# Performance work log

Measured on AMD Instinct MI355X. Metric: run time of the kernel, lower is better.

Reference implementation:

```python
import jax, jax.numpy as jnp
import numpy as np

ROUTING_ITERS = 3
EPS = 1e-8


def squash(x):
    # scale = ||x||^2 / (1 + ||x||^2); out = scale * x / (||x|| + eps)
    norm = jnp.linalg.norm(x, axis=-1, keepdims=True)
    scale = norm ** 2 / (1.0 + norm ** 2)
    return scale * x / (norm + EPS)


def setup_inputs() -> dict:
    key = jax.random.key(0)
    kx, kw = jax.random.split(key)
    B, R, C, IC, OC = 256, 1152, 10, 8, 16
    x = jax.random.normal(kx, (B, R, IC), dtype=jnp.float32)
    # learned prediction weights: [1, num_routes, num_capsules, in_ch, out_ch]
    weights = jax.random.normal(kw, (1, R, C, IC, OC), dtype=jnp.float32)
    return {"x": x, "weights": weights}


def reference(x, weights):
    # prediction vectors u_hat[b,r,c,o] = sum_i x[b,r,i] * W[r,c,i,o]
    u = jnp.einsum('bri,rcio->brco', x, weights[0])  # [B,R,C,OC]
    b = jnp.zeros(u.shape[:3], dtype=u.dtype)        # routing logits [B,R,C]
    v = jnp.zeros(u.shape[:1] + u.shape[2:], dtype=u.dtype)
    for _ in range(ROUTING_ITERS):
        c = jax.nn.softmax(b, axis=-1)               # coupling coeffs over capsules
        s = jnp.einsum('brc,brco->bco', c, u)        # weighted sum over routes
        v = squash(s)                                # [B,C,OC]
        b = b + jnp.einsum('brco,bco->brc', u, v)    # agreement update
    return v
```

## Files before the change

kernel.cpp:

```cpp
#include <hip/hip_runtime.h>
#include <cstdint>
#include <cstddef>

#define NB 256
#define NR 1152
#define NC 10
#define NI 8
#define NO 16
#define NSPLIT 2
#define NSWEEP 9
#define NRC 144

static __device__ __forceinline__ uint32_t bf16_pack2(float lo, float hi) {
    uint32_t vl = __float_as_uint(lo);
    vl = vl + 0x7FFFu + ((vl >> 16) & 1u);
    uint32_t vh = __float_as_uint(hi);
    vh = vh + 0x7FFFu + ((vh >> 16) & 1u);
    return (vl >> 16) | (vh & 0xFFFF0000u);
}

__global__ __launch_bounds__(320, 2) void caps_u_s1_kernel(
    const float* __restrict__ x, const float* __restrict__ W,
    uint32_t* __restrict__ u, uint32_t* __restrict__ part1)
{
    const int t  = threadIdx.x;
    const int c  = t >> 5;
    const int rl = (t & 31) >> 2;
    const int oq = t & 3;
    const int rc = blockIdx.x >> 4;
    const int bg = blockIdx.x & 15;
    const int b0 = bg * 16;
    const int r  = rc * 8 + rl;

    __shared__ float xs[16][8][8];

    if (t < 256) {
        const int bi = t >> 4, rem = t & 15;
        const int rr = rem >> 1, hf = rem & 1;
        *(float4*)&xs[bi][rr][hf * 4] =
            *(const float4*)(x + ((size_t)(b0 + bi) * NR + rc * 8 + rr) * 8 + hf * 4);
    }

    const float* wb = W + ((size_t)r * NC + c) * (NI * NO) + oq * 4;
    float4 wf[8];
#pragma unroll
    for (int i = 0; i < 8; ++i) wf[i] = *(const float4*)(wb + i * NO);

    __syncthreads();

#pragma unroll 2
    for (int bi = 0; bi < 16; ++bi) {
        const float4 xv4a = *(const float4*)&xs[bi][rl][0];
        const float4 xv4b = *(const float4*)&xs[bi][rl][4];
        const float xr[8] = {xv4a.x, xv4a.y, xv4a.z, xv4a.w,
                             xv4b.x, xv4b.y, xv4b.z, xv4b.w};
        float ax = 0.f, ay = 0.f, az = 0.f, aw = 0.f;
#pragma unroll
        for (int i = 0; i < 8; ++i) {
            const float xv = xr[i];
            ax = fmaf(xv, wf[i].x, ax); ay = fmaf(xv, wf[i].y, ay);
            az = fmaf(xv, wf[i].z, az); aw = fmaf(xv, wf[i].w, aw);
        }
        uint2 s;
        s.x = bf16_pack2(ax, ay);
        s.y = bf16_pack2(az, aw);
        *(uint2*)(u + (((size_t)(b0 + bi) * NC + c) * NR + r) * 8 + oq * 2) = s;

        float sx = ax, sy = ay, sz = az, sw = aw;
#pragma unroll
        for (int off = 4; off <= 16; off <<= 1) {
            sx += __shfl_xor(sx, off); sy += __shfl_xor(sy, off);
            sz += __shfl_xor(sz, off); sw += __shfl_xor(sw, off);
        }
        if ((t & 28) == 0) {
            uint2 p;
            p.x = bf16_pack2(sx, sy);
            p.y = bf16_pack2(sz, sw);
            *(uint2*)(part1 + ((size_t)(b0 + bi) * NRC + rc) * 80
                      + c * 8 + oq * 2) = p;
        }
    }
}

static __device__ __forceinline__ float vsum1_col(
    const uint32_t* __restrict__ part1, const int b, const int t)
{
    const uint32_t* p = part1 + (size_t)b * NRC * 80 + (t >> 1);
    const bool hi = t & 1;
    float s0 = 0.f, s1 = 0.f, s2 = 0.f, s3 = 0.f;
#pragma unroll 4
    for (int g = 0; g < NRC; g += 4) {
        const uint32_t w0 = p[(g + 0) * 80];
        const uint32_t w1 = p[(g + 1) * 80];
        const uint32_t w2 = p[(g + 2) * 80];
        const uint32_t w3 = p[(g + 3) * 80];
        s0 += hi ? __uint_as_float(w0 & 0xFFFF0000u) : __uint_as_float(w0 << 16);
        s1 += hi ? __uint_as_float(w1 & 0xFFFF0000u) : __uint_as_float(w1 << 16);
        s2 += hi ? __uint_as_float(w2 & 0xFFFF0000u) : __uint_as_float(w2 << 16);
        s3 += hi ? __uint_as_float(w3 & 0xFFFF0000u) : __uint_as_float(w3 << 16);
    }
    const float s = 0.1f * ((s0 + s1) + (s2 + s3));
    float n2 = s * s;
    n2 += __shfl_xor(n2, 1);
    n2 += __shfl_xor(n2, 2);
    n2 += __shfl_xor(n2, 4);
    n2 += __shfl_xor(n2, 8);
    const float nrm   = sqrtf(n2);
    return s * (n2 / (1.f + n2) / (nrm + 1e-8f));
}

__global__ __launch_bounds__(256, 2) void caps_pass_kernel(
    const uint32_t* __restrict__ u, const uint32_t* __restrict__ part1,
    const float* __restrict__ part_prev, float* __restrict__ partout)
{
    const int b  = blockIdx.x >> 1;
    const int sp = blockIdx.x & 1;
    const int t  = threadIdx.x;
    const int oq = t & 3;
    const int rl = t >> 2;

    __shared__ float vss[160];
    __shared__ float sred[4][160];

    if (t < 160) {
        float v = vsum1_col(part1, b, t);
        if (part_prev != nullptr) {
            const float s = part_prev[(size_t)b * 160 + t]
                          + part_prev[((size_t)NB + b) * 160 + t];
            float n2 = s * s;
            n2 += __shfl_xor(n2, 1);
            n2 += __shfl_xor(n2, 2);
            n2 += __shfl_xor(n2, 4);
            n2 += __shfl_xor(n2, 8);
            const float nrm = sqrtf(n2);
            v += s * (n2 / (1.f + n2) / (nrm + 1e-8f));
        }
        vss[t] = v;
    }
    __syncthreads();

    float acc[10][4];
#pragma unroll
    for (int c = 0; c < 10; ++c)
#pragma unroll
        for (int j = 0; j < 4; ++j) acc[c][j] = 0.f;

    const uint2* ub = (const uint2*)u + (size_t)b * NC * NR * 4 + oq;

    for (int k = 0; k < NSWEEP; ++k) {
        const int r = sp * (NSWEEP * 64) + k * 64 + rl;
        uint2 q[10];
#pragma unroll
        for (int c = 0; c < 10; ++c) q[c] = ub[((size_t)c * NR + r) * 4];

        float lg[10];
#pragma unroll
        for (int c = 0; c < 10; ++c) {
            const float4 vq = *(const float4*)&vss[c * 16 + oq * 4];
            float d = __uint_as_float(q[c].x << 16) * vq.x;
            d = fmaf(__uint_as_float(q[c].x & 0xFFFF0000u), vq.y, d);
            d = fmaf(__uint_as_float(q[c].y << 16),         vq.z, d);
            d = fmaf(__uint_as_float(q[c].y & 0xFFFF0000u), vq.w, d);
            lg[c] = d;
        }
#pragma unroll
        for (int c = 0; c < 10; ++c) {
            lg[c] += __shfl_xor(lg[c], 1);
            lg[c] += __shfl_xor(lg[c], 2);
        }
        float m = lg[0];
#pragma unroll
        for (int c = 1; c < 10; ++c) m = fmaxf(m, lg[c]);
        float wgt[10], ssum = 0.f;
#pragma unroll
        for (int c = 0; c < 10; ++c) { wgt[c] = __expf(lg[c] - m); ssum += wgt[c]; }
        const float inv = 1.f / ssum;
#pragma unroll
        for (int c = 0; c < 10; ++c) {
            const float wv = wgt[c] * inv;
            acc[c][0] = fmaf(wv, __uint_as_float(q[c].x << 16),         acc[c][0]);
            acc[c][1] = fmaf(wv, __uint_as_float(q[c].x & 0xFFFF0000u), acc[c][1]);
            acc[c][2] = fmaf(wv, __uint_as_float(q[c].y << 16),         acc[c][2]);
            acc[c][3] = fmaf(wv, __uint_as_float(q[c].y & 0xFFFF0000u), acc[c][3]);
        }
    }

#pragma unroll
    for (int off = 4; off <= 32; off <<= 1)
#pragma unroll
        for (int c = 0; c < 10; ++c)
#pragma unroll
            for (int j = 0; j < 4; ++j) acc[c][j] += __shfl_xor(acc[c][j], off);

    const int wv = t >> 6;
    if ((t & 63) < 4) {
#pragma unroll
        for (int c = 0; c < 10; ++c)
#pragma unroll
            for (int j = 0; j < 4; ++j)
                sred[wv][c * 16 + oq * 4 + j] = acc[c][j];
    }
    __syncthreads();

    if (t < 160) {
        partout[((size_t)sp * NB + b) * 160 + t]
            = sred[0][t] + sred[1][t] + sred[2][t] + sred[3][t];
    }
}

__global__ __launch_bounds__(192) void caps_final_kernel(
    const float* __restrict__ part2b, float* __restrict__ out)
{
    const int b = blockIdx.x;
    const int t = threadIdx.x;
    if (t >= 160) return;
    const float s = part2b[(size_t)b * 160 + t]
                  + part2b[((size_t)NB + b) * 160 + t];
    float n2 = s * s;
    n2 += __shfl_xor(n2, 1);
    n2 += __shfl_xor(n2, 2);
    n2 += __shfl_xor(n2, 4);
    n2 += __shfl_xor(n2, 8);
    const float nrm   = sqrtf(n2);
    const float scale = n2 / (1.f + n2) / (nrm + 1e-8f);
    out[(size_t)b * 160 + t] = scale * s;
}

extern "C" void kernel_launch(void* const* d_in, const int* in_sizes, int n_in,
                              void* d_out, int out_size, void* d_ws, size_t ws_size,
                              hipStream_t stream) {
    const float* x = (const float*)d_in[0];
    const float* W = (const float*)d_in[1];
    float* out = (float*)d_out;

    uint8_t*  ws   = (uint8_t*)d_ws;
    uint32_t* u    = (uint32_t*)ws;
    uint32_t* prt1 = (uint32_t*)(ws + 94371840u);
    float*    p2a  = (float*)(ws + 94371840u + 11796480u);
    float*    p2b  = (float*)(ws + 94371840u + 11796480u + 327680u);

    caps_u_s1_kernel<<<2304, 320, 0, stream>>>(x, W, u, prt1);
    caps_pass_kernel<<<NB * NSPLIT, 256, 0, stream>>>(u, prt1, nullptr, p2a);
    caps_pass_kernel<<<NB * NSPLIT, 256, 0, stream>>>(u, prt1, p2a, p2b);
    caps_final_kernel<<<NB, 192, 0, stream>>>(p2b, out);
}
```

Measured before the change: 142.8 us.

## Split routing passes six ways per batch and stage u slice in LDS

The routing pass kernels now split each batch's 1152 routes across six blocks of 192 routes instead of two blocks of 576. Each block first bulk-loads its bf16 u slice into shared memory with wide vector loads, then reads it from LDS in the sweep loop. This raises the block count to improve GPU fill and latency hiding on the memory-bound passes. In exchange it adds 60KB of LDS per block, which limits occupancy, and triples the partial-sum reduction work in the consumers.

```diff
diff --git a/kernel.cpp b/kernel.cpp
--- a/kernel.cpp
+++ b/kernel.cpp
@@ -7,8 +7,8 @@
 #define NC 10
 #define NI 8
 #define NO 16
-#define NSPLIT 2
-#define NSWEEP 9
+#define NSPLIT 6
+#define RPB 192
 #define NRC 144
 
 static __device__ __forceinline__ uint32_t bf16_pack2(float lo, float hi) {
@@ -105,7 +105,7 @@
     n2 += __shfl_xor(n2, 2);
     n2 += __shfl_xor(n2, 4);
     n2 += __shfl_xor(n2, 8);
-    const float nrm   = sqrtf(n2);
+    const float nrm = sqrtf(n2);
     return s * (n2 / (1.f + n2) / (nrm + 1e-8f));
 }
 
@@ -113,20 +113,35 @@
     const uint32_t* __restrict__ u, const uint32_t* __restrict__ part1,
     const float* __restrict__ part_prev, float* __restrict__ partout)
 {
-    const int b  = blockIdx.x >> 1;
-    const int sp = blockIdx.x & 1;
+    const int b  = blockIdx.x / NSPLIT;
+    const int sp = blockIdx.x % NSPLIT;
     const int t  = threadIdx.x;
     const int oq = t & 3;
     const int rl = t >> 2;
 
+    __shared__ uint32_t lds_u[15360];
     __shared__ float vss[160];
     __shared__ float sred[4][160];
+
+    {
+        const uint4* gsrc = (const uint4*)u;
+#pragma unroll
+        for (int j = 0; j < 15; ++j) {
+            const int f  = j * 256 + t;
+            const int c  = f / 384;
+            const int ro = f - c * 384;
+            const uint4 v = gsrc[((size_t)(b * NC + c) * NR + sp * RPB) * 2 + ro];
+            *(uint4*)&lds_u[(size_t)f * 4] = v;
+        }
+    }
 
     if (t < 160) {
         float v = vsum1_col(part1, b, t);
         if (part_prev != nullptr) {
-            const float s = part_prev[(size_t)b * 160 + t]
-                          + part_prev[((size_t)NB + b) * 160 + t];
+            float s = 0.f;
+#pragma unroll
+            for (int sp2 = 0; sp2 < NSPLIT; ++sp2)
+                s += part_prev[((size_t)sp2 * NB + b) * 160 + t];
             float n2 = s * s;
             n2 += __shfl_xor(n2, 1);
             n2 += __shfl_xor(n2, 2);
@@ -145,13 +160,12 @@
 #pragma unroll
         for (int j = 0; j < 4; ++j) acc[c][j] = 0.f;
 
-    const uint2* ub = (const uint2*)u + (size_t)b * NC * NR * 4 + oq;
-
-    for (int k = 0; k < NSWEEP; ++k) {
-        const int r = sp * (NSWEEP * 64) + k * 64 + rl;
+    for (int k = 0; k < 3; ++k) {
+        const int r = k * 64 + rl;
         uint2 q[10];
 #pragma unroll
-        for (int c = 0; c < 10; ++c) q[c] = ub[((size_t)c * NR + r) * 4];
+        for (int c = 0; c < 10; ++c)
+            q[c] = *(const uint2*)&lds_u[c * 1536 + r * 8 + oq * 2];
 
         float lg[10];
 #pragma unroll
@@ -214,8 +228,10 @@
     const int b = blockIdx.x;
     const int t = threadIdx.x;
     if (t >= 160) return;
-    const float s = part2b[(size_t)b * 160 + t]
-                  + part2b[((size_t)NB + b) * 160 + t];
+    float s = 0.f;
+#pragma unroll
+    for (int sp = 0; sp < NSPLIT; ++sp)
+        s += part2b[((size_t)sp * NB + b) * 160 + t];
     float n2 = s * s;
     n2 += __shfl_xor(n2, 1);
     n2 += __shfl_xor(n2, 2);
@@ -237,7 +253,7 @@
     uint32_t* u    = (uint32_t*)ws;
     uint32_t* prt1 = (uint32_t*)(ws + 94371840u);
     float*    p2a  = (float*)(ws + 94371840u + 11796480u);
-    float*    p2b  = (float*)(ws + 94371840u + 11796480u + 327680u);
+    float*    p2b  = (float*)(ws + 94371840u + 11796480u + 983040u);
 
     caps_u_s1_kernel<<<2304, 320, 0, stream>>>(x, W, u, prt1);
     caps_pass_kernel<<<NB * NSPLIT, 256, 0, stream>>>(u, prt1, nullptr, p2a);
```

Result: slower. 182.4 us (+27.7%).
